# Performance work log

Measured on AMD Instinct MI355X. Metric: run time of the kernel, lower is better.

The kernel has to match this reference:

```python
import jax, jax.numpy as jnp
import numpy as np

OUT_DIM = 1024


def setup_inputs() -> dict:
    key = jax.random.key(0)
    k1, k2, k3, k4 = jax.random.split(key, 4)
    B, N, D = 4, 2048, 1024
    s = 1.0 / np.sqrt(D)
    return {
        "x": jax.random.normal(k1, (B, N, D), dtype=jnp.float32),
        "W_query": jax.random.normal(k2, (D, OUT_DIM), dtype=jnp.float32) * s,
        "W_key": jax.random.normal(k3, (D, OUT_DIM), dtype=jnp.float32) * s,
        "W_value": jax.random.normal(k4, (D, OUT_DIM), dtype=jnp.float32) * s,
    }


def reference(x, W_query, W_key, W_value):
    # x: [B, N, D_in]; W_*: [D_in, D_out] (torch Linear weight transposed)
    q = jnp.einsum("bnd,de->bne", x, W_query)
    k = jnp.einsum("bnd,de->bne", x, W_key)
    v = jnp.einsum("bnd,de->bne", x, W_value)
    sqrt_d = jnp.sqrt(jnp.asarray(OUT_DIM, dtype=jnp.float32))
    scores = jnp.einsum("bie,bje->bij", q, k) / sqrt_d  # [B, N, N]
    # NOTE: original uses softmax over dim=1 (query axis), not the usual dim=2
    attn = jax.nn.softmax(scores, axis=1)
    # dropout with train=False is identity (eval-mode reference)
    # out = attn^T @ v  ->  out[b, j] = sum_i attn[b, i, j] * v[b, i]
    return jnp.einsum("bij,bie->bje", attn, v)
```

## Files before the change

kernel.cpp:

```cpp
#include <hip/hip_runtime.h>
#include <math.h>


typedef __bf16 bf16x8 __attribute__((ext_vector_type(8)));
typedef float f32x4 __attribute__((ext_vector_type(4)));

static __device__ __forceinline__ unsigned short f2bf(float f) {
    unsigned u = __float_as_uint(f);
    u += 0x7fff + ((u >> 16) & 1);
    return (unsigned short)(u >> 16);
}

#define GLDS16(gptr, lptr)                                                            \
    __builtin_amdgcn_global_load_lds(                                                 \
        (const __attribute__((address_space(1))) void*)(gptr),                        \
        (__attribute__((address_space(3))) void*)(lptr), 16, 0, 0)

#define BARSYNC  __builtin_amdgcn_s_barrier()
#define WAITLGKM do { asm volatile("s_waitcnt lgkmcnt(0)" ::: "memory");    \
                      __builtin_amdgcn_sched_barrier(0); } while (0)

__device__ __forceinline__ void gemm256_core(
    const unsigned short* __restrict__ Ab,
    const unsigned short* __restrict__ Bb,
    const long ld, unsigned short* lds, f32x4 acc[8][4])
{
    const int tid  = threadIdx.x;
    const int w    = tid >> 6;
    const int lane = tid & 63;

    const int r  = lane >> 3;
    const int s  = lane & 7;
    const int cg = (s ^ r) * 8;

    const int fr    = lane & 15;
    const int quad  = lane >> 4;
    const int sw    = fr & 7;
    const int arow0 = (w >> 2) * 128;
    const int brow0 = (w & 3) * 64;

#define STG_A(t, mh, buf) do {                                              \
    const int rb_ = (w >> 2) * 128 + (mh) * 64 + (w & 3) * 16;              \
    const unsigned short* g_ = Ab + (long)(rb_ + r) * ld + (long)(t) * 64 + cg; \
    unsigned short* d_ = lds + (buf) * 16384 + rb_ * 64;                    \
    GLDS16(g_, d_); GLDS16(g_ + 8 * ld, d_ + 512); } while (0)
#define STG_B(t, nh, buf) do {                                              \
    const int rb_ = (w >> 1) * 64 + (nh) * 32 + (w & 1) * 16;               \
    const unsigned short* g_ = Bb + (long)(rb_ + r) * ld + (long)(t) * 64 + cg; \
    unsigned short* d_ = lds + 32768 + (buf) * 16384 + rb_ * 64;            \
    GLDS16(g_, d_); GLDS16(g_ + 8 * ld, d_ + 512); } while (0)

    bf16x8 af[4][2], bfA[2][2], bfB[2][2];
#define LOADA(buf, mh) do {                                                 \
    _Pragma("unroll") for (int ks_ = 0; ks_ < 2; ks_++)                     \
    _Pragma("unroll") for (int i_ = 0; i_ < 4; i_++)                        \
        af[i_][ks_] = *(const bf16x8*)&lds[(buf) * 16384 +                  \
            (arow0 + (mh) * 64 + i_ * 16 + fr) * 64 +                       \
            ((ks_ * 4 + quad) ^ sw) * 8]; } while (0)
#define LOADB(BF, buf, nh) do {                                             \
    _Pragma("unroll") for (int ks_ = 0; ks_ < 2; ks_++)                     \
    _Pragma("unroll") for (int j_ = 0; j_ < 2; j_++)                        \
        BF[j_][ks_] = *(const bf16x8*)&lds[32768 + (buf) * 16384 +          \
            (brow0 + (nh) * 32 + j_ * 16 + fr) * 64 +                       \
            ((ks_ * 4 + quad) ^ sw) * 8]; } while (0)

#define MFMA16(mh, nh, BF) do {                                             \
    __builtin_amdgcn_s_setprio(1);                                          \
    _Pragma("unroll") for (int ks_ = 0; ks_ < 2; ks_++)                     \
    _Pragma("unroll") for (int i_ = 0; i_ < 4; i_++)                        \
    _Pragma("unroll") for (int j_ = 0; j_ < 2; j_++)                        \
        acc[(mh) * 4 + i_][(nh) * 2 + j_] =                                 \
            __builtin_amdgcn_mfma_f32_16x16x32_bf16(                        \
                af[i_][ks_], BF[j_][ks_],                                   \
                acc[(mh) * 4 + i_][(nh) * 2 + j_], 0, 0, 0);                \
    __builtin_amdgcn_s_setprio(0); } while (0)

#pragma unroll
    for (int i = 0; i < 8; i++)
#pragma unroll
        for (int j = 0; j < 4; j++) acc[i][j] = f32x4{0.f, 0.f, 0.f, 0.f};

    STG_A(0, 0, 0); STG_A(0, 1, 0); STG_B(0, 0, 0); STG_B(0, 1, 0);
    STG_A(1, 0, 1); STG_B(1, 1, 1);
    asm volatile("s_waitcnt vmcnt(4)" ::: "memory");
    BARSYNC;

#pragma unroll 1
    for (int i = 0; i < 8; ++i) {
        const int t1 = 2 * i + 1;
        const int t2 = (2 * i + 2) & 15;
        const int t3 = (2 * i + 3) & 15;
        LOADA(0, 0); LOADB(bfA, 0, 0); STG_B(t1, 0, 1);
        BARSYNC; WAITLGKM; MFMA16(0, 0, bfA); BARSYNC;
        LOADB(bfB, 0, 1); STG_A(t1, 1, 1);
        BARSYNC; WAITLGKM; MFMA16(0, 1, bfB); BARSYNC;
        LOADA(0, 1); STG_A(t2, 0, 0);
        BARSYNC; WAITLGKM; MFMA16(1, 1, bfB); BARSYNC;
        STG_B(t2, 1, 0);
        BARSYNC; MFMA16(1, 0, bfA);
        asm volatile("s_waitcnt vmcnt(4)" ::: "memory"); BARSYNC;
        LOADA(1, 0); LOADB(bfA, 1, 0); STG_A(t2, 1, 0);
        BARSYNC; WAITLGKM; MFMA16(0, 0, bfA); BARSYNC;
        LOADB(bfB, 1, 1); STG_B(t2, 0, 0);
        BARSYNC; WAITLGKM; MFMA16(0, 1, bfB); BARSYNC;
        LOADA(1, 1); STG_A(t3, 0, 1);
        BARSYNC; WAITLGKM; MFMA16(1, 1, bfB); BARSYNC;
        STG_B(t3, 1, 1);
        BARSYNC; MFMA16(1, 0, bfA);
        asm volatile("s_waitcnt vmcnt(4)" ::: "memory"); BARSYNC;
    }
    asm volatile("s_waitcnt vmcnt(0)" ::: "memory");

#undef STG_A
#undef STG_B
#undef LOADA
#undef LOADB
#undef MFMA16
}

__device__ __forceinline__ void gemm_v128_core(
    const unsigned short* __restrict__ Ab,
    const unsigned short* __restrict__ Bb,
    unsigned short* lds, f32x4 acc[4][4])
{
    const int tid  = threadIdx.x;
    const int w    = tid >> 6;
    const int lane = tid & 63;

    const int r  = lane >> 3;
    const int s  = lane & 7;
    const int cg = (s ^ r) * 8;

    const int fr    = lane & 15;
    const int quad  = lane >> 4;
    const int sw    = fr & 7;
    const int arow0 = (w >> 2) * 64;
    const int brow0 = (w & 3) * 64;

#define STG_VA(t, mh, buf) do {                                             \
    const int rb_ = (w >> 2) * 64 + (mh) * 32 + (w & 3) * 8;                \
    const unsigned short* g_ = Ab + (long)(rb_ + r) * 1024 + (long)(t) * 64 + cg; \
    unsigned short* d_ = lds + (buf) * 8192 + rb_ * 64;                     \
    GLDS16(g_, d_); } while (0)
#define STG_VB(t, nh, buf) do {                                             \
    const int rb_ = (w >> 1) * 64 + (nh) * 32 + (w & 1) * 16;               \
    const unsigned short* g_ = Bb + (long)(rb_ + r) * 1024 + (long)(t) * 64 + cg; \
    unsigned short* d_ = lds + 16384 + (buf) * 16384 + rb_ * 64;            \
    GLDS16(g_, d_); GLDS16(g_ + 8 * 1024, d_ + 512); } while (0)

    bf16x8 af[2][2], bfA[2][2], bfB[2][2];
#define LOADVA(buf, mh) do {                                                \
    _Pragma("unroll") for (int ks_ = 0; ks_ < 2; ks_++)                     \
    _Pragma("unroll") for (int i_ = 0; i_ < 2; i_++)                        \
        af[i_][ks_] = *(const bf16x8*)&lds[(buf) * 8192 +                   \
            (arow0 + (mh) * 32 + i_ * 16 + fr) * 64 +                       \
            ((ks_ * 4 + quad) ^ sw) * 8]; } while (0)
#define LOADVB(BF, buf, nh) do {                                            \
    _Pragma("unroll") for (int ks_ = 0; ks_ < 2; ks_++)                     \
    _Pragma("unroll") for (int j_ = 0; j_ < 2; j_++)                        \
        BF[j_][ks_] = *(const bf16x8*)&lds[16384 + (buf) * 16384 +          \
            (brow0 + (nh) * 32 + j_ * 16 + fr) * 64 +                       \
            ((ks_ * 4 + quad) ^ sw) * 8]; } while (0)

#define MFMA_V(mh, nh, BF) do {                                             \
    __builtin_amdgcn_s_setprio(1);                                          \
    _Pragma("unroll") for (int ks_ = 0; ks_ < 2; ks_++)                     \
    _Pragma("unroll") for (int i_ = 0; i_ < 2; i_++)                        \
    _Pragma("unroll") for (int j_ = 0; j_ < 2; j_++)                        \
        acc[(mh) * 2 + i_][(nh) * 2 + j_] =                                 \
            __builtin_amdgcn_mfma_f32_16x16x32_bf16(                        \
                af[i_][ks_], BF[j_][ks_],                                   \
                acc[(mh) * 2 + i_][(nh) * 2 + j_], 0, 0, 0);                \
    __builtin_amdgcn_s_setprio(0); } while (0)

#pragma unroll
    for (int i = 0; i < 4; i++)
#pragma unroll
        for (int j = 0; j < 4; j++) acc[i][j] = f32x4{0.f, 0.f, 0.f, 0.f};

    STG_VA(0, 0, 0); STG_VA(0, 1, 0); STG_VB(0, 0, 0); STG_VB(0, 1, 0);
    STG_VA(1, 0, 1); STG_VB(1, 1, 1);
    asm volatile("s_waitcnt vmcnt(3)" ::: "memory");
    BARSYNC;

#pragma unroll 1
    for (int i = 0; i < 8; ++i) {
        const int t1 = 2 * i + 1;
        const int t2 = (2 * i + 2) & 15;
        const int t3 = (2 * i + 3) & 15;
        LOADVA(0, 0); LOADVB(bfA, 0, 0); STG_VB(t1, 0, 1);
        BARSYNC; WAITLGKM; MFMA_V(0, 0, bfA); BARSYNC;
        LOADVB(bfB, 0, 1); STG_VA(t1, 1, 1);
        BARSYNC; WAITLGKM; MFMA_V(0, 1, bfB); BARSYNC;
        LOADVA(0, 1); STG_VA(t2, 0, 0);
        BARSYNC; WAITLGKM; MFMA_V(1, 1, bfB); BARSYNC;
        STG_VB(t2, 1, 0);
        BARSYNC; MFMA_V(1, 0, bfA);
        asm volatile("s_waitcnt vmcnt(3)" ::: "memory"); BARSYNC;
        LOADVA(1, 0); LOADVB(bfA, 1, 0); STG_VA(t2, 1, 0);
        BARSYNC; WAITLGKM; MFMA_V(0, 0, bfA); BARSYNC;
        LOADVB(bfB, 1, 1); STG_VB(t2, 0, 0);
        BARSYNC; WAITLGKM; MFMA_V(0, 1, bfB); BARSYNC;
        LOADVA(1, 1); STG_VA(t3, 0, 1);
        BARSYNC; WAITLGKM; MFMA_V(1, 1, bfB); BARSYNC;
        STG_VB(t3, 1, 1);
        BARSYNC; MFMA_V(1, 0, bfA);
        asm volatile("s_waitcnt vmcnt(3)" ::: "memory"); BARSYNC;
    }
    asm volatile("s_waitcnt vmcnt(0)" ::: "memory");

#undef STG_VA
#undef STG_VB
#undef LOADVA
#undef LOADVB
#undef MFMA_V
}

__device__ __forceinline__ void pv256_core(
    const unsigned short* __restrict__ Ab,
    const unsigned short* __restrict__ Bb,
    unsigned short* lds, f32x4 acc[8][2])
{
    const int tid  = threadIdx.x;
    const int w    = tid >> 6;
    const int lane = tid & 63;

    const int r  = lane >> 3;
    const int s  = lane & 7;
    const int cg = (s ^ r) * 8;

    const int fr    = lane & 15;
    const int quad  = lane >> 4;
    const int sw    = fr & 7;
    const int arow0 = (w >> 2) * 128;
    const int brow0 = (w & 3) * 32;

#define STG_PA(t, mh, buf) do {                                             \
    const int rb_ = (w >> 2) * 128 + (mh) * 64 + (w & 3) * 16;              \
    const unsigned short* g_ = Ab + (long)(rb_ + r) * 2048 + (long)(t) * 64 + cg; \
    unsigned short* d_ = lds + (buf) * 16384 + rb_ * 64;                    \
    GLDS16(g_, d_); GLDS16(g_ + 8 * 2048, d_ + 512); } while (0)
#define STG_PB(t, nh, buf) do {                                             \
    const int rb_ = (w & 3) * 32 + (nh) * 16 + (w >> 2) * 8;                \
    const unsigned short* g_ = Bb + (long)(rb_ + r) * 8192 + (long)(t) * 64 + cg; \
    unsigned short* d_ = lds + 32768 + (buf) * 8192 + rb_ * 64;             \
    GLDS16(g_, d_); } while (0)

    bf16x8 af[4][2], bfA[2], bfB[2];
#define LOADPA(buf, mh) do {                                                \
    _Pragma("unroll") for (int ks_ = 0; ks_ < 2; ks_++)                     \
    _Pragma("unroll") for (int i_ = 0; i_ < 4; i_++)                        \
        af[i_][ks_] = *(const bf16x8*)&lds[(buf) * 16384 +                  \
            (arow0 + (mh) * 64 + i_ * 16 + fr) * 64 +                       \
            ((ks_ * 4 + quad) ^ sw) * 8]; } while (0)
#define LOADPB(BF, buf, nh) do {                                            \
    _Pragma("unroll") for (int ks_ = 0; ks_ < 2; ks_++)                     \
        BF[ks_] = *(const bf16x8*)&lds[32768 + (buf) * 8192 +               \
            (brow0 + (nh) * 16 + fr) * 64 +                                 \
            ((ks_ * 4 + quad) ^ sw) * 8]; } while (0)

#define MFMA8(mh, nh, BF) do {                                              \
    __builtin_amdgcn_s_setprio(1);                                          \
    _Pragma("unroll") for (int ks_ = 0; ks_ < 2; ks_++)                     \
    _Pragma("unroll") for (int i_ = 0; i_ < 4; i_++)                        \
        acc[(mh) * 4 + i_][nh] = __builtin_amdgcn_mfma_f32_16x16x32_bf16(   \
            af[i_][ks_], BF[ks_], acc[(mh) * 4 + i_][nh], 0, 0, 0);         \
    __builtin_amdgcn_s_setprio(0); } while (0)

#pragma unroll
    for (int i = 0; i < 8; i++)
#pragma unroll
        for (int j = 0; j < 2; j++) acc[i][j] = f32x4{0.f, 0.f, 0.f, 0.f};

    STG_PA(0, 0, 0); STG_PA(0, 1, 0); STG_PB(0, 0, 0); STG_PB(0, 1, 0);
    STG_PA(1, 0, 1); STG_PB(1, 1, 1);
    asm volatile("s_waitcnt vmcnt(3)" ::: "memory");
    BARSYNC;

#pragma unroll 1
    for (int i = 0; i < 16; ++i) {
        const int t1 = 2 * i + 1;
        const int t2 = (2 * i + 2) & 31;
        const int t3 = (2 * i + 3) & 31;
        LOADPA(0, 0); LOADPB(bfA, 0, 0); STG_PB(t1, 0, 1);
        BARSYNC; WAITLGKM; MFMA8(0, 0, bfA); BARSYNC;
        LOADPB(bfB, 0, 1); STG_PA(t1, 1, 1);
        BARSYNC; WAITLGKM; MFMA8(0, 1, bfB); BARSYNC;
        LOADPA(0, 1); STG_PA(t2, 0, 0);
        BARSYNC; WAITLGKM; MFMA8(1, 1, bfB); BARSYNC;
        STG_PB(t2, 1, 0);
        BARSYNC; MFMA8(1, 0, bfA);
        asm volatile("s_waitcnt vmcnt(3)" ::: "memory"); BARSYNC;
        LOADPA(1, 0); LOADPB(bfA, 1, 0); STG_PA(t2, 1, 0);
        BARSYNC; WAITLGKM; MFMA8(0, 0, bfA); BARSYNC;
        LOADPB(bfB, 1, 1); STG_PB(t2, 0, 0);
        BARSYNC; WAITLGKM; MFMA8(0, 1, bfB); BARSYNC;
        LOADPA(1, 1); STG_PA(t3, 0, 1);
        BARSYNC; WAITLGKM; MFMA8(1, 1, bfB); BARSYNC;
        STG_PB(t3, 1, 1);
        BARSYNC; MFMA8(1, 0, bfA);
        asm volatile("s_waitcnt vmcnt(3)" ::: "memory"); BARSYNC;
    }
    asm volatile("s_waitcnt vmcnt(0)" ::: "memory");

#undef STG_PA
#undef STG_PB
#undef LOADPA
#undef LOADPB
#undef MFMA8
}

__global__ __launch_bounds__(512, 2) void gemm_qk256(
    const unsigned short* __restrict__ X, const unsigned short* __restrict__ W,
    unsigned short* __restrict__ QK)
{
    __shared__ unsigned short lds[65536];
    const int orig = blockIdx.x;
    const int xcd  = orig & 7;
    const int pos  = orig >> 3;
    const long gm0 = (long)(pos >> 2) * 256;
    const long gn0 = (long)(xcd * 4 + (pos & 3)) * 256;

    f32x4 acc[8][4];
    gemm256_core(W + gm0 * 1024, X + gn0 * 1024, 1024, lds, acc);

    const int tid = threadIdx.x;
    const int w = tid >> 6, lane = tid & 63;
    const int fr = lane & 15, quad = lane >> 4;
    const int wm = (w >> 2) * 128, wn = (w & 3) * 64;

#pragma unroll
    for (int mi = 0; mi < 8; mi++) {
        const long rb = gm0 + wm + (mi >> 2) * 64 + (mi & 3) * 16 + quad * 4;
#pragma unroll
        for (int n = 0; n < 4; n++) {
            const long cb = gn0 + wn + n * 16 + fr;
            ushort4 o;
            o.x = f2bf(acc[mi][n][0]);
            o.y = f2bf(acc[mi][n][1]);
            o.z = f2bf(acc[mi][n][2]);
            o.w = f2bf(acc[mi][n][3]);
            *(ushort4*)&QK[cb * 2048L + rb] = o;
        }
    }
}

__global__ __launch_bounds__(512, 2) void gemm_v128(
    const unsigned short* __restrict__ A, const unsigned short* __restrict__ B,
    unsigned short* __restrict__ Vt)
{
    __shared__ unsigned short lds[49152];
    const int orig = blockIdx.x;
    const int xcd  = orig & 7;
    const int pos  = orig >> 3;
    const long gm0 = (long)(xcd * 8 + (pos & 7)) * 128;
    const long gn0 = (long)(pos >> 3) * 256;

    f32x4 acc[4][4];
    gemm_v128_core(A + gm0 * 1024, B + gn0 * 1024, lds, acc);

    const int tid = threadIdx.x;
    const int w = tid >> 6, lane = tid & 63;
    const int fr = lane & 15, quad = lane >> 4;
    const int wm = (w >> 2) * 64, wn = (w & 3) * 64;

#pragma unroll
    for (int ai = 0; ai < 4; ai++) {
        const long rb = gm0 + wm + ai * 16 + quad * 4;
#pragma unroll
        for (int aj = 0; aj < 4; aj++) {
            const long ce = gn0 + wn + aj * 16 + fr;
            ushort4 o;
            o.x = f2bf(acc[ai][aj][0]);
            o.y = f2bf(acc[ai][aj][1]);
            o.z = f2bf(acc[ai][aj][2]);
            o.w = f2bf(acc[ai][aj][3]);
            *(ushort4*)&Vt[ce * 8192L + rb] = o;
        }
    }
}

__global__ __launch_bounds__(512, 2) void gemm_scores256(
    const unsigned short* __restrict__ QKb, unsigned short* __restrict__ P,
    float* __restrict__ l)
{
    __shared__ unsigned short lds[65536];
    const int orig = blockIdx.x;
    const int xcd  = orig & 7;
    const int pos  = orig >> 3;
    const int bz   = xcd >> 1;
    const long gm0 = (long)((xcd & 1) * 4 + (pos >> 3)) * 256;
    const long gn0 = (long)(pos & 7) * 256;

    const unsigned short* Ab = QKb + (long)bz * 2048 * 2048 + gm0 * 2048;
    const unsigned short* Bb = QKb + (long)bz * 2048 * 2048 + 1024 + gn0 * 2048;

    f32x4 acc[8][4];
    gemm256_core(Ab, Bb, 2048, lds, acc);

    const int tid = threadIdx.x;
    const int w = tid >> 6, lane = tid & 63;
    const int fr = lane & 15, quad = lane >> 4;
    const int wm = (w >> 2) * 128, wn = (w & 3) * 64;

    unsigned short* Pb = P + (long)bz * 2048 * 2048;
    float* lb = l + (long)bz * 2048;
    const float scale = 1.0f / 32.0f;

    float colsum[4] = {0.f, 0.f, 0.f, 0.f};
#pragma unroll
    for (int mi = 0; mi < 8; mi++) {
        const long rb = gm0 + wm + (mi >> 2) * 64 + (mi & 3) * 16 + quad * 4;
#pragma unroll
        for (int n = 0; n < 4; n++) {
            const long cb = gn0 + wn + n * 16 + fr;
            float e0 = __expf(acc[mi][n][0] * scale);
            float e1 = __expf(acc[mi][n][1] * scale);
            float e2 = __expf(acc[mi][n][2] * scale);
            float e3 = __expf(acc[mi][n][3] * scale);
            colsum[n] += (e0 + e1) + (e2 + e3);
            ushort4 o;
            o.x = f2bf(e0); o.y = f2bf(e1); o.z = f2bf(e2); o.w = f2bf(e3);
            *(ushort4*)&Pb[cb * 2048L + rb] = o;
        }
    }
#pragma unroll
    for (int n = 0; n < 4; n++) {
        colsum[n] += __shfl_xor(colsum[n], 16);
        colsum[n] += __shfl_xor(colsum[n], 32);
    }
    if (quad == 0) {
#pragma unroll
        for (int n = 0; n < 4; n++)
            atomicAdd(&lb[gn0 + wn + n * 16 + fr], colsum[n]);
    }
}

__global__ __launch_bounds__(512, 2) void gemm_pv256(
    const unsigned short* __restrict__ P, const unsigned short* __restrict__ Vt,
    const float* __restrict__ l, float* __restrict__ out)
{
    __shared__ unsigned short lds[49152];
    const int orig = blockIdx.x;
    const int xcd  = orig & 7;
    const int pos  = orig >> 3;
    const int bz   = xcd >> 1;
    const long gm0 = (long)((xcd & 1) * 4 + (pos >> 3)) * 256;
    const long gn0 = (long)(pos & 7) * 128;

    const unsigned short* Ab = P + (long)bz * 2048 * 2048 + gm0 * 2048;
    const unsigned short* Bb = Vt + gn0 * 8192 + (long)bz * 2048;

    f32x4 acc[8][2];
    pv256_core(Ab, Bb, lds, acc);

    const int tid = threadIdx.x;
    const int w = tid >> 6, lane = tid & 63;
    const int fr = lane & 15, quad = lane >> 4;
    const int wm = (w >> 2) * 128, wn = (w & 3) * 32;

    float* Ob = out + (long)bz * 2048 * 1024;
    const float* lb = l + (long)bz * 2048;
#pragma unroll
    for (int mi = 0; mi < 8; mi++) {
        const long rb = gm0 + wm + (mi >> 2) * 64 + (mi & 3) * 16 + quad * 4;
        float inv[4];
#pragma unroll
        for (int rr = 0; rr < 4; rr++) inv[rr] = 1.0f / lb[rb + rr];
#pragma unroll
        for (int nj = 0; nj < 2; nj++) {
            const long cb = gn0 + wn + nj * 16 + fr;
#pragma unroll
            for (int rr = 0; rr < 4; rr++)
                Ob[(rb + rr) * 1024L + cb] = acc[mi][nj][rr] * inv[rr];
        }
    }
}

__global__ __launch_bounds__(256) void prep(
    const float* __restrict__ x,
    const float* __restrict__ Wq, const float* __restrict__ Wk,
    const float* __restrict__ Wv,
    unsigned short* __restrict__ xb, unsigned short* __restrict__ Wqkvt,
    float* __restrict__ l)
{
    __shared__ float t[32][33];
    const int b = blockIdx.x;
    const int tid = threadIdx.x;
    if (b < 8192) {
        int i = b * 256 + tid;
        float4 v = ((const float4*)x)[i];
        ushort4 o;
        o.x = f2bf(v.x); o.y = f2bf(v.y); o.z = f2bf(v.z); o.w = f2bf(v.w);
        ((ushort4*)xb)[i] = o;
        return;
    }
    if (b == 8192 + 3072) {
        float4 z = {0.f, 0.f, 0.f, 0.f};
#pragma unroll
        for (int i = 0; i < 8; i++)
            ((float4*)l)[tid * 8 + i] = z;
        return;
    }
    int tix = b - 8192;
    const int w = tix >> 10;
    tix &= 1023;
    const float* W = (w == 0) ? Wq : (w == 1) ? Wk : Wv;
    unsigned short* Wt = Wqkvt + (long)w * 1024 * 1024;
    const int bx = (tix & 31) * 32;
    const int by = (tix >> 5) * 32;
    const int tx = tid & 31;
    const int ty = (tid >> 5) * 4;
#pragma unroll
    for (int j = 0; j < 4; j++)
        t[ty + j][tx] = W[(long)(by + ty + j) * 1024 + bx + tx];
    __syncthreads();
#pragma unroll
    for (int j = 0; j < 4; j++)
        Wt[(long)(bx + ty + j) * 1024 + by + tx] = f2bf(t[tx][ty + j]);
}

extern "C" void kernel_launch(void* const* d_in, const int* in_sizes, int n_in,
                              void* d_out, int out_size, void* d_ws,
                              size_t ws_size, hipStream_t stream)
{
    const float* x  = (const float*)d_in[0];
    const float* Wq = (const float*)d_in[1];
    const float* Wk = (const float*)d_in[2];
    const float* Wv = (const float*)d_in[3];
    float* out = (float*)d_out;

    const long M1 = 1024 * 1024;
    unsigned short* u     = (unsigned short*)d_ws;
    unsigned short* xb    = u;
    unsigned short* Wqkvt = u + 8 * M1;
    unsigned short* QKb   = Wqkvt + 3 * M1;
    unsigned short* Vtb   = QKb + 16 * M1;
    unsigned short* Pb    = Vtb + 8 * M1;
    float* l              = (float*)(Pb + 16 * M1);

    prep<<<dim3(8192 + 3072 + 1), dim3(256), 0, stream>>>(x, Wq, Wk, Wv, xb, Wqkvt, l);

    gemm_qk256<<<dim3(256), dim3(512), 0, stream>>>(xb, Wqkvt, QKb);

    gemm_v128<<<dim3(256), dim3(512), 0, stream>>>(xb, Wqkvt + 2 * M1, Vtb);

    gemm_scores256<<<dim3(256), dim3(512), 0, stream>>>(QKb, Pb, l);

    gemm_pv256<<<dim3(256), dim3(512), 0, stream>>>(Pb, Vtb, l, out);
}
```

Measured before the change: 217.2 us.

## Merge QK and V projection launches and retile PV GEMM to 128x128

Combines the QK and V projection GEMMs into one kernel launch that branches on block index, removing a launch and the tail between the two. Retiles the attention-times-V GEMM from 256x128 tiles with 512 threads to 128x128 tiles with 256 threads, doubling the block count for better occupancy and load balance. The smaller tiles reduce operand reuse per block and add global traffic.

Result: slower. 222.2 us (+2.3%).

```diff
diff --git a/kernel.cpp b/kernel.cpp
--- a/kernel.cpp
+++ b/kernel.cpp
@@ -216,10 +216,10 @@
 #undef MFMA_V
 }
 
-__device__ __forceinline__ void pv256_core(
+__device__ __forceinline__ void pv128_core(
     const unsigned short* __restrict__ Ab,
     const unsigned short* __restrict__ Bb,
-    unsigned short* lds, f32x4 acc[8][2])
+    unsigned short* lds, f32x4 acc[4][4])
 {
     const int tid  = threadIdx.x;
     const int w    = tid >> 6;
@@ -232,49 +232,53 @@
     const int fr    = lane & 15;
     const int quad  = lane >> 4;
     const int sw    = fr & 7;
-    const int arow0 = (w >> 2) * 128;
-    const int brow0 = (w & 3) * 32;
-
-#define STG_PA(t, mh, buf) do {                                             \
-    const int rb_ = (w >> 2) * 128 + (mh) * 64 + (w & 3) * 16;              \
+    const int arow0 = (w >> 1) * 64;
+    const int brow0 = (w & 1) * 64;
+
+#define STG_QA(t, mh, buf) do {                                             \
+    const int rb_ = (w >> 1) * 64 + (mh) * 32 + (w & 1) * 16;               \
     const unsigned short* g_ = Ab + (long)(rb_ + r) * 2048 + (long)(t) * 64 + cg; \
-    unsigned short* d_ = lds + (buf) * 16384 + rb_ * 64;                    \
+    unsigned short* d_ = lds + (buf) * 8192 + rb_ * 64;                     \
     GLDS16(g_, d_); GLDS16(g_ + 8 * 2048, d_ + 512); } while (0)
-#define STG_PB(t, nh, buf) do {                                             \
-    const int rb_ = (w & 3) * 32 + (nh) * 16 + (w >> 2) * 8;                \
+#define STG_QB(t, nh, buf) do {                                             \
+    const int rb_ = (w & 1) * 64 + (nh) * 32 + (w >> 1) * 16;               \
     const unsigned short* g_ = Bb + (long)(rb_ + r) * 8192 + (long)(t) * 64 + cg; \
-    unsigned short* d_ = lds + 32768 + (buf) * 8192 + rb_ * 64;             \
-    GLDS16(g_, d_); } while (0)
-
-    bf16x8 af[4][2], bfA[2], bfB[2];
-#define LOADPA(buf, mh) do {                                                \
-    _Pragma("unroll") for (int ks_ = 0; ks_ < 2; ks_++)                     \
-    _Pragma("unroll") for (int i_ = 0; i_ < 4; i_++)                        \
-        af[i_][ks_] = *(const bf16x8*)&lds[(buf) * 16384 +                  \
-            (arow0 + (mh) * 64 + i_ * 16 + fr) * 64 +                       \
+    unsigned short* d_ = lds + 16384 + (buf) * 8192 + rb_ * 64;             \
+    GLDS16(g_, d_); GLDS16(g_ + 8 * 8192, d_ + 512); } while (0)
+
+    bf16x8 af[2][2], bfA[2][2], bfB[2][2];
+#define LOADQA(buf, mh) do {                                                \
+    _Pragma("unroll") for (int ks_ = 0; ks_ < 2; ks_++)                     \
+    _Pragma("unroll") for (int i_ = 0; i_ < 2; i_++)                        \
+        af[i_][ks_] = *(const bf16x8*)&lds[(buf) * 8192 +                   \
+            (arow0 + (mh) * 32 + i_ * 16 + fr) * 64 +                       \
             ((ks_ * 4 + quad) ^ sw) * 8]; } while (0)
-#define LOADPB(BF, buf, nh) do {                                            \
-    _Pragma("unroll") for (int ks_ = 0; ks_ < 2; ks_++)                     \
-        BF[ks_] = *(const bf16x8*)&lds[32768 + (buf) * 8192 +               \
-            (brow0 + (nh) * 16 + fr) * 64 +                                 \
+#define LOADQB(BF, buf, nh) do {                                            \
+    _Pragma("unroll") for (int ks_ = 0; ks_ < 2; ks_++)                     \
+    _Pragma("unroll") for (int j_ = 0; j_ < 2; j_++)                        \
+        BF[j_][ks_] = *(const bf16x8*)&lds[16384 + (buf) * 8192 +           \
+            (brow0 + (nh) * 32 + j_ * 16 + fr) * 64 +                       \
             ((ks_ * 4 + quad) ^ sw) * 8]; } while (0)
 
-#define MFMA8(mh, nh, BF) do {                                              \
+#define MFMA_Q(mh, nh, BF) do {                                             \
     __builtin_amdgcn_s_setprio(1);                                          \
     _Pragma("unroll") for (int ks_ = 0; ks_ < 2; ks_++)                     \
-    _Pragma("unroll") for (int i_ = 0; i_ < 4; i_++)                        \
-        acc[(mh) * 4 + i_][nh] = __builtin_amdgcn_mfma_f32_16x16x32_bf16(   \
-            af[i_][ks_], BF[ks_], acc[(mh) * 4 + i_][nh], 0, 0, 0);         \
+    _Pragma("unroll") for (int i_ = 0; i_ < 2; i_++)                        \
+    _Pragma("unroll") for (int j_ = 0; j_ < 2; j_++)                        \
+        acc[(mh) * 2 + i_][(nh) * 2 + j_] =                                 \
+            __builtin_amdgcn_mfma_f32_16x16x32_bf16(                        \
+                af[i_][ks_], BF[j_][ks_],                                   \
+                acc[(mh) * 2 + i_][(nh) * 2 + j_], 0, 0, 0);                \
     __builtin_amdgcn_s_setprio(0); } while (0)
 
 #pragma unroll
-    for (int i = 0; i < 8; i++)
-#pragma unroll
-        for (int j = 0; j < 2; j++) acc[i][j] = f32x4{0.f, 0.f, 0.f, 0.f};
-
-    STG_PA(0, 0, 0); STG_PA(0, 1, 0); STG_PB(0, 0, 0); STG_PB(0, 1, 0);
-    STG_PA(1, 0, 1); STG_PB(1, 1, 1);
-    asm volatile("s_waitcnt vmcnt(3)" ::: "memory");
+    for (int i = 0; i < 4; i++)
+#pragma unroll
+        for (int j = 0; j < 4; j++) acc[i][j] = f32x4{0.f, 0.f, 0.f, 0.f};
+
+    STG_QA(0, 0, 0); STG_QA(0, 1, 0); STG_QB(0, 0, 0); STG_QB(0, 1, 0);
+    STG_QA(1, 0, 1); STG_QB(1, 1, 1);
+    asm volatile("s_waitcnt vmcnt(4)" ::: "memory");
     BARSYNC;
 
 #pragma unroll 1
@@ -282,100 +286,92 @@
         const int t1 = 2 * i + 1;
         const int t2 = (2 * i + 2) & 31;
         const int t3 = (2 * i + 3) & 31;
-        LOADPA(0, 0); LOADPB(bfA, 0, 0); STG_PB(t1, 0, 1);
-        BARSYNC; WAITLGKM; MFMA8(0, 0, bfA); BARSYNC;
-        LOADPB(bfB, 0, 1); STG_PA(t1, 1, 1);
-        BARSYNC; WAITLGKM; MFMA8(0, 1, bfB); BARSYNC;
-        LOADPA(0, 1); STG_PA(t2, 0, 0);
-        BARSYNC; WAITLGKM; MFMA8(1, 1, bfB); BARSYNC;
-        STG_PB(t2, 1, 0);
-        BARSYNC; MFMA8(1, 0, bfA);
-        asm volatile("s_waitcnt vmcnt(3)" ::: "memory"); BARSYNC;
-        LOADPA(1, 0); LOADPB(bfA, 1, 0); STG_PA(t2, 1, 0);
-        BARSYNC; WAITLGKM; MFMA8(0, 0, bfA); BARSYNC;
-        LOADPB(bfB, 1, 1); STG_PB(t2, 0, 0);
-        BARSYNC; WAITLGKM; MFMA8(0, 1, bfB); BARSYNC;
-        LOADPA(1, 1); STG_PA(t3, 0, 1);
-        BARSYNC; WAITLGKM; MFMA8(1, 1, bfB); BARSYNC;
-        STG_PB(t3, 1, 1);
-        BARSYNC; MFMA8(1, 0, bfA);
-        asm volatile("s_waitcnt vmcnt(3)" ::: "memory"); BARSYNC;
+        LOADQA(0, 0); LOADQB(bfA, 0, 0); STG_QB(t1, 0, 1);
+        BARSYNC; WAITLGKM; MFMA_Q(0, 0, bfA); BARSYNC;
+        LOADQB(bfB, 0, 1); STG_QA(t1, 1, 1);
+        BARSYNC; WAITLGKM; MFMA_Q(0, 1, bfB); BARSYNC;
+        LOADQA(0, 1); STG_QA(t2, 0, 0);
+        BARSYNC; WAITLGKM; MFMA_Q(1, 1, bfB); BARSYNC;
+        STG_QB(t2, 1, 0);
+        BARSYNC; MFMA_Q(1, 0, bfA);
+        asm volatile("s_waitcnt vmcnt(4)" ::: "memory"); BARSYNC;
+        LOADQA(1, 0); LOADQB(bfA, 1, 0); STG_QA(t2, 1, 0);
+        BARSYNC; WAITLGKM; MFMA_Q(0, 0, bfA); BARSYNC;
+        LOADQB(bfB, 1, 1); STG_QB(t2, 0, 0);
+        BARSYNC; WAITLGKM; MFMA_Q(0, 1, bfB); BARSYNC;
+        LOADQA(1, 1); STG_QA(t3, 0, 1);
+        BARSYNC; WAITLGKM; MFMA_Q(1, 1, bfB); BARSYNC;
+        STG_QB(t3, 1, 1);
+        BARSYNC; MFMA_Q(1, 0, bfA);
+        asm volatile("s_waitcnt vmcnt(4)" ::: "memory"); BARSYNC;
     }
     asm volatile("s_waitcnt vmcnt(0)" ::: "memory");
 
-#undef STG_PA
-#undef STG_PB
-#undef LOADPA
-#undef LOADPB
-#undef MFMA8
-}
-
-__global__ __launch_bounds__(512, 2) void gemm_qk256(
+#undef STG_QA
+#undef STG_QB
+#undef LOADQA
+#undef LOADQB
+#undef MFMA_Q
+}
+
+__global__ __launch_bounds__(512, 2) void gemm_qkv_split(
     const unsigned short* __restrict__ X, const unsigned short* __restrict__ W,
-    unsigned short* __restrict__ QK)
+    unsigned short* __restrict__ QK, unsigned short* __restrict__ Vt)
 {
     __shared__ unsigned short lds[65536];
-    const int orig = blockIdx.x;
-    const int xcd  = orig & 7;
-    const int pos  = orig >> 3;
-    const long gm0 = (long)(pos >> 2) * 256;
-    const long gn0 = (long)(xcd * 4 + (pos & 3)) * 256;
-
-    f32x4 acc[8][4];
-    gemm256_core(W + gm0 * 1024, X + gn0 * 1024, 1024, lds, acc);
-
     const int tid = threadIdx.x;
     const int w = tid >> 6, lane = tid & 63;
     const int fr = lane & 15, quad = lane >> 4;
-    const int wm = (w >> 2) * 128, wn = (w & 3) * 64;
-
-#pragma unroll
-    for (int mi = 0; mi < 8; mi++) {
-        const long rb = gm0 + wm + (mi >> 2) * 64 + (mi & 3) * 16 + quad * 4;
-#pragma unroll
-        for (int n = 0; n < 4; n++) {
-            const long cb = gn0 + wn + n * 16 + fr;
-            ushort4 o;
-            o.x = f2bf(acc[mi][n][0]);
-            o.y = f2bf(acc[mi][n][1]);
-            o.z = f2bf(acc[mi][n][2]);
-            o.w = f2bf(acc[mi][n][3]);
-            *(ushort4*)&QK[cb * 2048L + rb] = o;
+
+    if (blockIdx.x < 256) {
+        const int orig = blockIdx.x;
+        const int xcd  = orig & 7;
+        const int pos  = orig >> 3;
+        const long gm0 = (long)(pos >> 2) * 256;
+        const long gn0 = (long)(xcd * 4 + (pos & 3)) * 256;
+
+        f32x4 acc[8][4];
+        gemm256_core(W + gm0 * 1024, X + gn0 * 1024, 1024, lds, acc);
+
+        const int wm = (w >> 2) * 128, wn = (w & 3) * 64;
+#pragma unroll
+        for (int mi = 0; mi < 8; mi++) {
+            const long rb = gm0 + wm + (mi >> 2) * 64 + (mi & 3) * 16 + quad * 4;
+#pragma unroll
+            for (int n = 0; n < 4; n++) {
+                const long cb = gn0 + wn + n * 16 + fr;
+                ushort4 o;
+                o.x = f2bf(acc[mi][n][0]);
+                o.y = f2bf(acc[mi][n][1]);
+                o.z = f2bf(acc[mi][n][2]);
+                o.w = f2bf(acc[mi][n][3]);
+                *(ushort4*)&QK[cb * 2048L + rb] = o;
+            }
         }
-    }
-}
-
-__global__ __launch_bounds__(512, 2) void gemm_v128(
-    const unsigned short* __restrict__ A, const unsigned short* __restrict__ B,
-    unsigned short* __restrict__ Vt)
-{
-    __shared__ unsigned short lds[49152];
-    const int orig = blockIdx.x;
-    const int xcd  = orig & 7;
-    const int pos  = orig >> 3;
-    const long gm0 = (long)(xcd * 8 + (pos & 7)) * 128;
-    const long gn0 = (long)(pos >> 3) * 256;
-
-    f32x4 acc[4][4];
-    gemm_v128_core(A + gm0 * 1024, B + gn0 * 1024, lds, acc);
-
-    const int tid = threadIdx.x;
-    const int w = tid >> 6, lane = tid & 63;
-    const int fr = lane & 15, quad = lane >> 4;
-    const int wm = (w >> 2) * 64, wn = (w & 3) * 64;
-
-#pragma unroll
-    for (int ai = 0; ai < 4; ai++) {
-        const long rb = gm0 + wm + ai * 16 + quad * 4;
-#pragma unroll
-        for (int aj = 0; aj < 4; aj++) {
-            const long ce = gn0 + wn + aj * 16 + fr;
-            ushort4 o;
-            o.x = f2bf(acc[ai][aj][0]);
-            o.y = f2bf(acc[ai][aj][1]);
-            o.z = f2bf(acc[ai][aj][2]);
-            o.w = f2bf(acc[ai][aj][3]);
-            *(ushort4*)&Vt[ce * 8192L + rb] = o;
+    } else {
+        const int orig = blockIdx.x - 256;
+        const int xcd  = orig & 7;
+        const int pos  = orig >> 3;
+        const long gm0 = (long)(xcd * 8 + (pos & 7)) * 128;
+        const long gn0 = (long)(pos >> 3) * 256;
+
+        f32x4 acc[4][4];
+        gemm_v128_core(X + gm0 * 1024, W + 2 * 1024 * 1024L + gn0 * 1024, lds, acc);
+
+        const int wm = (w >> 2) * 64, wn = (w & 3) * 64;
+#pragma unroll
+        for (int ai = 0; ai < 4; ai++) {
+            const long rb = gm0 + wm + ai * 16 + quad * 4;
+#pragma unroll
+            for (int aj = 0; aj < 4; aj++) {
+                const long ce = gn0 + wn + aj * 16 + fr;
+                ushort4 o;
+                o.x = f2bf(acc[ai][aj][0]);
+                o.y = f2bf(acc[ai][aj][1]);
+                o.z = f2bf(acc[ai][aj][2]);
+                o.w = f2bf(acc[ai][aj][3]);
+                *(ushort4*)&Vt[ce * 8192L + rb] = o;
+            }
         }
     }
 }
@@ -436,43 +432,43 @@
     }
 }
 
-__global__ __launch_bounds__(512, 2) void gemm_pv256(
+__global__ __launch_bounds__(256, 2) void gemm_pv128(
     const unsigned short* __restrict__ P, const unsigned short* __restrict__ Vt,
     const float* __restrict__ l, float* __restrict__ out)
 {
-    __shared__ unsigned short lds[49152];
+    __shared__ unsigned short lds[32768];
     const int orig = blockIdx.x;
     const int xcd  = orig & 7;
     const int pos  = orig >> 3;
     const int bz   = xcd >> 1;
-    const long gm0 = (long)((xcd & 1) * 4 + (pos >> 3)) * 256;
+    const long gm0 = (long)((xcd & 1) * 8 + (pos >> 3)) * 128;
     const long gn0 = (long)(pos & 7) * 128;
 
     const unsigned short* Ab = P + (long)bz * 2048 * 2048 + gm0 * 2048;
     const unsigned short* Bb = Vt + gn0 * 8192 + (long)bz * 2048;
 
-    f32x4 acc[8][2];
-    pv256_core(Ab, Bb, lds, acc);
+    f32x4 acc[4][4];
+    pv128_core(Ab, Bb, lds, acc);
 
     const int tid = threadIdx.x;
     const int w = tid >> 6, lane = tid & 63;
     const int fr = lane & 15, quad = lane >> 4;
-    const int wm = (w >> 2) * 128, wn = (w & 3) * 32;
+    const int wm = (w >> 1) * 64, wn = (w & 1) * 64;
 
     float* Ob = out + (long)bz * 2048 * 1024;
     const float* lb = l + (long)bz * 2048;
 #pragma unroll
-    for (int mi = 0; mi < 8; mi++) {
-        const long rb = gm0 + wm + (mi >> 2) * 64 + (mi & 3) * 16 + quad * 4;
+    for (int ai = 0; ai < 4; ai++) {
+        const long rb = gm0 + wm + ai * 16 + quad * 4;
         float inv[4];
 #pragma unroll
         for (int rr = 0; rr < 4; rr++) inv[rr] = 1.0f / lb[rb + rr];
 #pragma unroll
-        for (int nj = 0; nj < 2; nj++) {
-            const long cb = gn0 + wn + nj * 16 + fr;
+        for (int aj = 0; aj < 4; aj++) {
+            const long cb = gn0 + wn + aj * 16 + fr;
 #pragma unroll
             for (int rr = 0; rr < 4; rr++)
-                Ob[(rb + rr) * 1024L + cb] = acc[mi][nj][rr] * inv[rr];
+                Ob[(rb + rr) * 1024L + cb] = acc[ai][aj][rr] * inv[rr];
         }
     }
 }
@@ -541,11 +537,9 @@
 
     prep<<<dim3(8192 + 3072 + 1), dim3(256), 0, stream>>>(x, Wq, Wk, Wv, xb, Wqkvt, l);
 
-    gemm_qk256<<<dim3(256), dim3(512), 0, stream>>>(xb, Wqkvt, QKb);
-
-    gemm_v128<<<dim3(256), dim3(512), 0, stream>>>(xb, Wqkvt + 2 * M1, Vtb);
+    gemm_qkv_split<<<dim3(512), dim3(512), 0, stream>>>(xb, Wqkvt, QKb, Vtb);
 
     gemm_scores256<<<dim3(256), dim3(512), 0, stream>>>(QKb, Pb, l);
 
-    gemm_pv256<<<dim3(256), dim3(512), 0, stream>>>(Pb, Vtb, l, out);
-}
+    gemm_pv128<<<dim3(512), dim3(256), 0, stream>>>(Pb, Vtb, l, out);
+}
```

## Fuse all attention stages into one cooperative persistent kernel with grid syncs

Applied to the files above, without the earlier changes.

Replaces the five separate launches (prep, QK projection, V projection, scores and PV GEMMs) with one cooperative kernel of 256 blocks that runs the stages in sequence, separated by grid-wide syncs. The prep work is spread across the persistent blocks, and the QK and V projections run back to back in each block. The aim is to remove per-launch overhead and pipeline drain gaps between kernels. In exchange it adds grid barrier cost, fixes the grid at 256 blocks with the larger LDS footprint for every stage, and may change occupancy.

Result: slower. 325.7 us (+50.0%).

```diff
diff --git a/kernel.cpp b/kernel.cpp
--- a/kernel.cpp
+++ b/kernel.cpp
@@ -1,5 +1,8 @@
 #include <hip/hip_runtime.h>
+#include <hip/hip_cooperative_groups.h>
 #include <math.h>
+
+namespace cg = cooperative_groups;
 
 
 typedef __bf16 bf16x8 __attribute__((ext_vector_type(8)));
@@ -310,214 +313,196 @@
 #undef MFMA8
 }
 
-__global__ __launch_bounds__(512, 2) void gemm_qk256(
-    const unsigned short* __restrict__ X, const unsigned short* __restrict__ W,
-    unsigned short* __restrict__ QK)
+__global__ __launch_bounds__(512, 2) void mega_attn(
+    const float* __restrict__ x,
+    const float* __restrict__ Wq, const float* __restrict__ Wk,
+    const float* __restrict__ Wv, float* __restrict__ out,
+    unsigned short* __restrict__ ws)
 {
     __shared__ unsigned short lds[65536];
-    const int orig = blockIdx.x;
-    const int xcd  = orig & 7;
-    const int pos  = orig >> 3;
-    const long gm0 = (long)(pos >> 2) * 256;
-    const long gn0 = (long)(xcd * 4 + (pos & 3)) * 256;
-
-    f32x4 acc[8][4];
-    gemm256_core(W + gm0 * 1024, X + gn0 * 1024, 1024, lds, acc);
-
+
+    const long M1 = 1024 * 1024;
+    unsigned short* xb    = ws;
+    unsigned short* Wqkvt = ws + 8 * M1;
+    unsigned short* QKb   = Wqkvt + 3 * M1;
+    unsigned short* Vtb   = QKb + 16 * M1;
+    unsigned short* Pb0   = Vtb + 8 * M1;
+    float* l              = (float*)(Pb0 + 16 * M1);
+
+    const int b   = blockIdx.x;
     const int tid = threadIdx.x;
     const int w = tid >> 6, lane = tid & 63;
     const int fr = lane & 15, quad = lane >> 4;
-    const int wm = (w >> 2) * 128, wn = (w & 3) * 64;
-
-#pragma unroll
-    for (int mi = 0; mi < 8; mi++) {
-        const long rb = gm0 + wm + (mi >> 2) * 64 + (mi & 3) * 16 + quad * 4;
+
+    cg::grid_group grid = cg::this_grid();
+
+    {
+        const float4* x4 = (const float4*)x;
+        ushort4* xb4 = (ushort4*)xb;
+#pragma unroll
+        for (int i = 0; i < 16; i++) {
+            const long idx = (long)i * (256 * 512) + (long)b * 512 + tid;
+            float4 v = x4[idx];
+            ushort4 o;
+            o.x = f2bf(v.x); o.y = f2bf(v.y); o.z = f2bf(v.z); o.w = f2bf(v.w);
+            xb4[idx] = o;
+        }
+        float* tf = (float*)lds;
+        const int sub = tid >> 8;
+        const int t2  = tid & 255;
+        const int tx  = t2 & 31;
+        const int ty  = (t2 >> 5) * 4;
+#pragma unroll 1
+        for (int stp = 0; stp < 6; stp++) {
+            const int tix = b * 12 + stp * 2 + sub;
+            const int wsel = tix >> 10;
+            const int t10  = tix & 1023;
+            const float* W = (wsel == 0) ? Wq : (wsel == 1) ? Wk : Wv;
+            unsigned short* Wt = Wqkvt + (long)wsel * M1;
+            const int bx = (t10 & 31) * 32;
+            const int by = (t10 >> 5) * 32;
+            float* tt = tf + sub * (32 * 33);
+#pragma unroll
+            for (int j = 0; j < 4; j++)
+                tt[(ty + j) * 33 + tx] = W[(long)(by + ty + j) * 1024 + bx + tx];
+            __syncthreads();
+#pragma unroll
+            for (int j = 0; j < 4; j++)
+                Wt[(long)(bx + ty + j) * 1024 + by + tx] = f2bf(tt[tx * 33 + ty + j]);
+            __syncthreads();
+        }
+        if (tid < 32) l[b * 32 + tid] = 0.f;
+    }
+    grid.sync();
+
+    {
+        const int xcd = b & 7;
+        const int pos = b >> 3;
+        {
+            const long gm0 = (long)(pos >> 2) * 256;
+            const long gn0 = (long)(xcd * 4 + (pos & 3)) * 256;
+            f32x4 acc[8][4];
+            gemm256_core(Wqkvt + gm0 * 1024, xb + gn0 * 1024, 1024, lds, acc);
+            const int wm = (w >> 2) * 128, wn = (w & 3) * 64;
+#pragma unroll
+            for (int mi = 0; mi < 8; mi++) {
+                const long rb = gm0 + wm + (mi >> 2) * 64 + (mi & 3) * 16 + quad * 4;
+#pragma unroll
+                for (int n = 0; n < 4; n++) {
+                    const long cb = gn0 + wn + n * 16 + fr;
+                    ushort4 o;
+                    o.x = f2bf(acc[mi][n][0]);
+                    o.y = f2bf(acc[mi][n][1]);
+                    o.z = f2bf(acc[mi][n][2]);
+                    o.w = f2bf(acc[mi][n][3]);
+                    *(ushort4*)&QKb[cb * 2048L + rb] = o;
+                }
+            }
+        }
+        __syncthreads();
+        {
+            const long gm0 = (long)(xcd * 8 + (pos & 7)) * 128;
+            const long gn0 = (long)(pos >> 3) * 256;
+            f32x4 acc[4][4];
+            gemm_v128_core(xb + gm0 * 1024, Wqkvt + 2 * M1 + gn0 * 1024, lds, acc);
+            const int wm = (w >> 2) * 64, wn = (w & 3) * 64;
+#pragma unroll
+            for (int ai = 0; ai < 4; ai++) {
+                const long rb = gm0 + wm + ai * 16 + quad * 4;
+#pragma unroll
+                for (int aj = 0; aj < 4; aj++) {
+                    const long ce = gn0 + wn + aj * 16 + fr;
+                    ushort4 o;
+                    o.x = f2bf(acc[ai][aj][0]);
+                    o.y = f2bf(acc[ai][aj][1]);
+                    o.z = f2bf(acc[ai][aj][2]);
+                    o.w = f2bf(acc[ai][aj][3]);
+                    *(ushort4*)&Vtb[ce * 8192L + rb] = o;
+                }
+            }
+        }
+    }
+    grid.sync();
+
+    {
+        const int xcd = b & 7;
+        const int pos = b >> 3;
+        const int bz  = xcd >> 1;
+        const long gm0 = (long)((xcd & 1) * 4 + (pos >> 3)) * 256;
+        const long gn0 = (long)(pos & 7) * 256;
+
+        const unsigned short* Ab = QKb + (long)bz * 2048 * 2048 + gm0 * 2048;
+        const unsigned short* Bb = QKb + (long)bz * 2048 * 2048 + 1024 + gn0 * 2048;
+
+        f32x4 acc[8][4];
+        gemm256_core(Ab, Bb, 2048, lds, acc);
+
+        const int wm = (w >> 2) * 128, wn = (w & 3) * 64;
+        unsigned short* Pb = Pb0 + (long)bz * 2048 * 2048;
+        float* lb = l + (long)bz * 2048;
+        const float scale = 1.0f / 32.0f;
+
+        float colsum[4] = {0.f, 0.f, 0.f, 0.f};
+#pragma unroll
+        for (int mi = 0; mi < 8; mi++) {
+            const long rb = gm0 + wm + (mi >> 2) * 64 + (mi & 3) * 16 + quad * 4;
+#pragma unroll
+            for (int n = 0; n < 4; n++) {
+                const long cb = gn0 + wn + n * 16 + fr;
+                float e0 = __expf(acc[mi][n][0] * scale);
+                float e1 = __expf(acc[mi][n][1] * scale);
+                float e2 = __expf(acc[mi][n][2] * scale);
+                float e3 = __expf(acc[mi][n][3] * scale);
+                colsum[n] += (e0 + e1) + (e2 + e3);
+                ushort4 o;
+                o.x = f2bf(e0); o.y = f2bf(e1); o.z = f2bf(e2); o.w = f2bf(e3);
+                *(ushort4*)&Pb[cb * 2048L + rb] = o;
+            }
+        }
 #pragma unroll
         for (int n = 0; n < 4; n++) {
-            const long cb = gn0 + wn + n * 16 + fr;
-            ushort4 o;
-            o.x = f2bf(acc[mi][n][0]);
-            o.y = f2bf(acc[mi][n][1]);
-            o.z = f2bf(acc[mi][n][2]);
-            o.w = f2bf(acc[mi][n][3]);
-            *(ushort4*)&QK[cb * 2048L + rb] = o;
-        }
-    }
-}
-
-__global__ __launch_bounds__(512, 2) void gemm_v128(
-    const unsigned short* __restrict__ A, const unsigned short* __restrict__ B,
-    unsigned short* __restrict__ Vt)
-{
-    __shared__ unsigned short lds[49152];
-    const int orig = blockIdx.x;
-    const int xcd  = orig & 7;
-    const int pos  = orig >> 3;
-    const long gm0 = (long)(xcd * 8 + (pos & 7)) * 128;
-    const long gn0 = (long)(pos >> 3) * 256;
-
-    f32x4 acc[4][4];
-    gemm_v128_core(A + gm0 * 1024, B + gn0 * 1024, lds, acc);
-
-    const int tid = threadIdx.x;
-    const int w = tid >> 6, lane = tid & 63;
-    const int fr = lane & 15, quad = lane >> 4;
-    const int wm = (w >> 2) * 64, wn = (w & 3) * 64;
-
-#pragma unroll
-    for (int ai = 0; ai < 4; ai++) {
-        const long rb = gm0 + wm + ai * 16 + quad * 4;
-#pragma unroll
-        for (int aj = 0; aj < 4; aj++) {
-            const long ce = gn0 + wn + aj * 16 + fr;
-            ushort4 o;
-            o.x = f2bf(acc[ai][aj][0]);
-            o.y = f2bf(acc[ai][aj][1]);
-            o.z = f2bf(acc[ai][aj][2]);
-            o.w = f2bf(acc[ai][aj][3]);
-            *(ushort4*)&Vt[ce * 8192L + rb] = o;
-        }
-    }
-}
-
-__global__ __launch_bounds__(512, 2) void gemm_scores256(
-    const unsigned short* __restrict__ QKb, unsigned short* __restrict__ P,
-    float* __restrict__ l)
-{
-    __shared__ unsigned short lds[65536];
-    const int orig = blockIdx.x;
-    const int xcd  = orig & 7;
-    const int pos  = orig >> 3;
-    const int bz   = xcd >> 1;
-    const long gm0 = (long)((xcd & 1) * 4 + (pos >> 3)) * 256;
-    const long gn0 = (long)(pos & 7) * 256;
-
-    const unsigned short* Ab = QKb + (long)bz * 2048 * 2048 + gm0 * 2048;
-    const unsigned short* Bb = QKb + (long)bz * 2048 * 2048 + 1024 + gn0 * 2048;
-
-    f32x4 acc[8][4];
-    gemm256_core(Ab, Bb, 2048, lds, acc);
-
-    const int tid = threadIdx.x;
-    const int w = tid >> 6, lane = tid & 63;
-    const int fr = lane & 15, quad = lane >> 4;
-    const int wm = (w >> 2) * 128, wn = (w & 3) * 64;
-
-    unsigned short* Pb = P + (long)bz * 2048 * 2048;
-    float* lb = l + (long)bz * 2048;
-    const float scale = 1.0f / 32.0f;
-
-    float colsum[4] = {0.f, 0.f, 0.f, 0.f};
-#pragma unroll
-    for (int mi = 0; mi < 8; mi++) {
-        const long rb = gm0 + wm + (mi >> 2) * 64 + (mi & 3) * 16 + quad * 4;
-#pragma unroll
-        for (int n = 0; n < 4; n++) {
-            const long cb = gn0 + wn + n * 16 + fr;
-            float e0 = __expf(acc[mi][n][0] * scale);
-            float e1 = __expf(acc[mi][n][1] * scale);
-            float e2 = __expf(acc[mi][n][2] * scale);
-            float e3 = __expf(acc[mi][n][3] * scale);
-            colsum[n] += (e0 + e1) + (e2 + e3);
-            ushort4 o;
-            o.x = f2bf(e0); o.y = f2bf(e1); o.z = f2bf(e2); o.w = f2bf(e3);
-            *(ushort4*)&Pb[cb * 2048L + rb] = o;
-        }
-    }
-#pragma unroll
-    for (int n = 0; n < 4; n++) {
-        colsum[n] += __shfl_xor(colsum[n], 16);
-        colsum[n] += __shfl_xor(colsum[n], 32);
-    }
-    if (quad == 0) {
-#pragma unroll
-        for (int n = 0; n < 4; n++)
-            atomicAdd(&lb[gn0 + wn + n * 16 + fr], colsum[n]);
-    }
-}
-
-__global__ __launch_bounds__(512, 2) void gemm_pv256(
-    const unsigned short* __restrict__ P, const unsigned short* __restrict__ Vt,
-    const float* __restrict__ l, float* __restrict__ out)
-{
-    __shared__ unsigned short lds[49152];
-    const int orig = blockIdx.x;
-    const int xcd  = orig & 7;
-    const int pos  = orig >> 3;
-    const int bz   = xcd >> 1;
-    const long gm0 = (long)((xcd & 1) * 4 + (pos >> 3)) * 256;
-    const long gn0 = (long)(pos & 7) * 128;
-
-    const unsigned short* Ab = P + (long)bz * 2048 * 2048 + gm0 * 2048;
-    const unsigned short* Bb = Vt + gn0 * 8192 + (long)bz * 2048;
-
-    f32x4 acc[8][2];
-    pv256_core(Ab, Bb, lds, acc);
-
-    const int tid = threadIdx.x;
-    const int w = tid >> 6, lane = tid & 63;
-    const int fr = lane & 15, quad = lane >> 4;
-    const int wm = (w >> 2) * 128, wn = (w & 3) * 32;
-
-    float* Ob = out + (long)bz * 2048 * 1024;
-    const float* lb = l + (long)bz * 2048;
-#pragma unroll
-    for (int mi = 0; mi < 8; mi++) {
-        const long rb = gm0 + wm + (mi >> 2) * 64 + (mi & 3) * 16 + quad * 4;
-        float inv[4];
-#pragma unroll
-        for (int rr = 0; rr < 4; rr++) inv[rr] = 1.0f / lb[rb + rr];
-#pragma unroll
-        for (int nj = 0; nj < 2; nj++) {
-            const long cb = gn0 + wn + nj * 16 + fr;
-#pragma unroll
-            for (int rr = 0; rr < 4; rr++)
-                Ob[(rb + rr) * 1024L + cb] = acc[mi][nj][rr] * inv[rr];
-        }
-    }
-}
-
-__global__ __launch_bounds__(256) void prep(
-    const float* __restrict__ x,
-    const float* __restrict__ Wq, const float* __restrict__ Wk,
-    const float* __restrict__ Wv,
-    unsigned short* __restrict__ xb, unsigned short* __restrict__ Wqkvt,
-    float* __restrict__ l)
-{
-    __shared__ float t[32][33];
-    const int b = blockIdx.x;
-    const int tid = threadIdx.x;
-    if (b < 8192) {
-        int i = b * 256 + tid;
-        float4 v = ((const float4*)x)[i];
-        ushort4 o;
-        o.x = f2bf(v.x); o.y = f2bf(v.y); o.z = f2bf(v.z); o.w = f2bf(v.w);
-        ((ushort4*)xb)[i] = o;
-        return;
-    }
-    if (b == 8192 + 3072) {
-        float4 z = {0.f, 0.f, 0.f, 0.f};
-#pragma unroll
-        for (int i = 0; i < 8; i++)
-            ((float4*)l)[tid * 8 + i] = z;
-        return;
-    }
-    int tix = b - 8192;
-    const int w = tix >> 10;
-    tix &= 1023;
-    const float* W = (w == 0) ? Wq : (w == 1) ? Wk : Wv;
-    unsigned short* Wt = Wqkvt + (long)w * 1024 * 1024;
-    const int bx = (tix & 31) * 32;
-    const int by = (tix >> 5) * 32;
-    const int tx = tid & 31;
-    const int ty = (tid >> 5) * 4;
-#pragma unroll
-    for (int j = 0; j < 4; j++)
-        t[ty + j][tx] = W[(long)(by + ty + j) * 1024 + bx + tx];
-    __syncthreads();
-#pragma unroll
-    for (int j = 0; j < 4; j++)
-        Wt[(long)(bx + ty + j) * 1024 + by + tx] = f2bf(t[tx][ty + j]);
+            colsum[n] += __shfl_xor(colsum[n], 16);
+            colsum[n] += __shfl_xor(colsum[n], 32);
+        }
+        if (quad == 0) {
+#pragma unroll
+            for (int n = 0; n < 4; n++)
+                atomicAdd(&lb[gn0 + wn + n * 16 + fr], colsum[n]);
+        }
+    }
+    grid.sync();
+
+    {
+        const int xcd = b & 7;
+        const int pos = b >> 3;
+        const int bz  = xcd >> 1;
+        const long gm0 = (long)((xcd & 1) * 4 + (pos >> 3)) * 256;
+        const long gn0 = (long)(pos & 7) * 128;
+
+        const unsigned short* Ab = Pb0 + (long)bz * 2048 * 2048 + gm0 * 2048;
+        const unsigned short* Bb = Vtb + gn0 * 8192 + (long)bz * 2048;
+
+        f32x4 acc[8][2];
+        pv256_core(Ab, Bb, lds, acc);
+
+        const int wm = (w >> 2) * 128, wn = (w & 3) * 32;
+        float* Ob = out + (long)bz * 2048 * 1024;
+        const float* lb = l + (long)bz * 2048;
+#pragma unroll
+        for (int mi = 0; mi < 8; mi++) {
+            const long rb = gm0 + wm + (mi >> 2) * 64 + (mi & 3) * 16 + quad * 4;
+            float inv[4];
+#pragma unroll
+            for (int rr = 0; rr < 4; rr++) inv[rr] = 1.0f / lb[rb + rr];
+#pragma unroll
+            for (int nj = 0; nj < 2; nj++) {
+                const long cb = gn0 + wn + nj * 16 + fr;
+#pragma unroll
+                for (int rr = 0; rr < 4; rr++)
+                    Ob[(rb + rr) * 1024L + cb] = acc[mi][nj][rr] * inv[rr];
+            }
+        }
+    }
 }
 
 extern "C" void kernel_launch(void* const* d_in, const int* in_sizes, int n_in,
@@ -529,23 +514,10 @@
     const float* Wk = (const float*)d_in[2];
     const float* Wv = (const float*)d_in[3];
     float* out = (float*)d_out;
-
-    const long M1 = 1024 * 1024;
-    unsigned short* u     = (unsigned short*)d_ws;
-    unsigned short* xb    = u;
-    unsigned short* Wqkvt = u + 8 * M1;
-    unsigned short* QKb   = Wqkvt + 3 * M1;
-    unsigned short* Vtb   = QKb + 16 * M1;
-    unsigned short* Pb    = Vtb + 8 * M1;
-    float* l              = (float*)(Pb + 16 * M1);
-
-    prep<<<dim3(8192 + 3072 + 1), dim3(256), 0, stream>>>(x, Wq, Wk, Wv, xb, Wqkvt, l);
-
-    gemm_qk256<<<dim3(256), dim3(512), 0, stream>>>(xb, Wqkvt, QKb);
-
-    gemm_v128<<<dim3(256), dim3(512), 0, stream>>>(xb, Wqkvt + 2 * M1, Vtb);
-
-    gemm_scores256<<<dim3(256), dim3(512), 0, stream>>>(QKb, Pb, l);
-
-    gemm_pv256<<<dim3(256), dim3(512), 0, stream>>>(Pb, Vtb, l, out);
+    unsigned short* u = (unsigned short*)d_ws;
+
+    void* args[] = {(void*)&x, (void*)&Wq, (void*)&Wk, (void*)&Wv,
+                    (void*)&out, (void*)&u};
+    hipLaunchCooperativeKernel((const void*)mega_attn, dim3(256), dim3(512),
+                               args, 0, stream);
 }
```
